# Kernel optimization log

Measured on AMD Instinct MI355X. Metric: run time of the kernel, lower is better.

Reference implementation:

```python
import jax, jax.numpy as jnp
import numpy as np

N_NODES = 19000   # STRING PPI nodes
N_EDGES = 600000  # avg degree ~32
B = 4096          # batch of perturbations
GNN = 256         # gnn_dim
H = 512           # hidden_dim
MID = 2048        # hidden_dim * expand
L = 6             # n_layers residual blocks
C = 3             # n_classes
R = 512           # bilinear_rank
G = 6640          # n_genes_out
LN_EPS = 1e-5


def _ln(x, scale, bias):
    mu = jnp.mean(x, axis=-1, keepdims=True)
    var = jnp.var(x, axis=-1, keepdims=True)
    return (x - mu) * jax.lax.rsqrt(var + LN_EPS) * scale + bias


def setup_inputs() -> dict:
    key = jax.random.key(0)
    ks = iter(jax.random.split(key, 24))
    s = lambda *sh: jax.random.normal(next(ks), sh, dtype=jnp.float32) * 0.02
    inp = {
        # -1 marks unknown genes (fallback embedding path)
        "node_indices": jax.random.randint(next(ks), (B,), -1, N_NODES),
        "edge_index": jax.random.randint(next(ks), (2, N_EDGES), 0, N_NODES),
        "edge_weight": jax.random.uniform(next(ks), (N_EDGES,), dtype=jnp.float32),
        # frozen mps.0-6 output cache (detached buffer in torch)
        "node_emb_cache": jax.random.normal(next(ks), (N_NODES, GNN), dtype=jnp.float32),
        # trainable graph tail (mps.7 modeled as GraphConv) + post_mp Linear
        "w_root": s(GNN, GNN),
        "w_neigh": s(GNN, GNN),
        "w_post": s(GNN, GNN),
        "b_post": jnp.zeros((GNN,), jnp.float32),
        "fallback_emb": s(GNN),
        # input_proj: LayerNorm(256) + Linear(256->512, no bias)
        "ln_in_scale": jnp.ones((GNN,), jnp.float32),
        "ln_in_bias": jnp.zeros((GNN,), jnp.float32),
        "w_in": s(H, GNN),
        # 6 residual blocks, stacked params
        "rb_ln_scale": jnp.ones((L, H), jnp.float32),
        "rb_ln_bias": jnp.zeros((L, H), jnp.float32),
        "rb_fc1": s(L, MID, H),
        "rb_fc2": s(L, H, MID),
        # bilinear head
        "w_bilinear": s(C * R, H),
        "out_gene_emb": s(G, R),
    }
    return inp


def reference(node_indices, edge_index, edge_weight, node_emb_cache,
              w_root, w_neigh, w_post, b_post, fallback_emb,
              ln_in_scale, ln_in_bias, w_in,
              rb_ln_scale, rb_ln_bias, rb_fc1, rb_fc2,
              w_bilinear, out_gene_emb):
    # --- trainable graph tail: mps.7 (GraphConv) + post_mp ---
    src, dst = edge_index[0], edge_index[1]
    msg = node_emb_cache[src] * edge_weight[:, None]          # [E, GNN]
    agg = jax.ops.segment_sum(msg, dst, num_segments=N_NODES)  # [N, GNN]
    x = jax.nn.relu(node_emb_cache @ w_root.T + agg @ w_neigh.T)
    node_emb = x @ w_post.T + b_post                           # [N, GNN]

    # --- gather perturbation embeddings with fallback for -1 ---
    known = node_indices >= 0
    safe = jnp.clip(node_indices, 0, None)
    pert = jnp.where(known[:, None], node_emb[safe], fallback_emb[None, :])  # [B, GNN]

    # --- input_proj + 6 residual blocks (dropout inactive in eval) ---
    h = _ln(pert, ln_in_scale, ln_in_bias) @ w_in.T            # [B, H]
    for i in range(L):
        y = _ln(h, rb_ln_scale[i], rb_ln_bias[i])
        y = jax.nn.gelu(y @ rb_fc1[i].T, approximate=False)    # exact erf GELU (torch default)
        h = y @ rb_fc2[i].T + h

    # --- bilinear head ---
    blin = (h @ w_bilinear.T).reshape(-1, C, R)                # [B, 3, R]
    logits = jnp.einsum('bcr,gr->bcg', blin, out_gene_emb)     # [B, 3, G]
    return logits
```

## Files before the change

kernel.cpp:

```cpp
#include <hip/hip_runtime.h>
#include <hip/hip_bf16.h>

#define N_NODES 19000
#define N_EDGES 600000
#define BATCH   4096
#define GNN_D   256
#define H_D     512
#define MID_D   2048
#define L_N     6
#define C_N     3
#define R_D     512
#define G_N     6640
#define LN_EPS  1e-5f
#define MAXDEG  128

typedef __attribute__((ext_vector_type(8))) short short8;
typedef __attribute__((ext_vector_type(4))) float f32x4;
typedef __hip_bfloat16 bf16;

#define SEG0 32768
#define SEG1 (SEG0 + 1572864)
#define SEG2 (SEG1 + 1572864)
#define SEG3 (SEG2 + 196608)
#define SEG4 (SEG3 + 849920)
#define SEG5 (SEG4 + 16384)
#define SEG6 (SEG5 + 32768)
#define CONV_TOT SEG6

__global__ void convert_weights_kernel(
    const float* __restrict__ w_in, const float* __restrict__ fc1,
    const float* __restrict__ fc2, const float* __restrict__ wbil,
    const float* __restrict__ gene, const float* __restrict__ wpost,
    const float* __restrict__ wroot, const float* __restrict__ wneigh,
    bf16* __restrict__ o_win, bf16* __restrict__ o_fc1, bf16* __restrict__ o_fc2,
    bf16* __restrict__ o_wbil, bf16* __restrict__ o_gene, bf16* __restrict__ o_wpost,
    bf16* __restrict__ o_wrn) {
  int i = blockIdx.x * blockDim.x + threadIdx.x;
  if (i >= CONV_TOT) return;
  const float* src;
  bf16* dst;
  if (i < SEG0)      { src = w_in  + (size_t)i * 4;            dst = o_win  + (size_t)i * 4; }
  else if (i < SEG1) { size_t j = i - SEG0; src = fc1  + j * 4; dst = o_fc1  + j * 4; }
  else if (i < SEG2) { size_t j = i - SEG1; src = fc2  + j * 4; dst = o_fc2  + j * 4; }
  else if (i < SEG3) { size_t j = i - SEG2; src = wbil + j * 4; dst = o_wbil + j * 4; }
  else if (i < SEG4) { size_t j = i - SEG3; src = gene + j * 4; dst = o_gene + j * 4; }
  else if (i < SEG5) { size_t j = i - SEG4; src = wpost+ j * 4; dst = o_wpost+ j * 4; }
  else {
    int j = i - SEG5;
    int base = j * 4;
    int n = base >> 9;
    int k = base & 511;
    src = (k < GNN_D) ? (wroot + (size_t)n * GNN_D + k)
                      : (wneigh + (size_t)n * GNN_D + (k - GNN_D));
    dst = o_wrn + base;
  }
  float4 v = *(const float4*)src;
  dst[0] = __float2bfloat16(v.x);
  dst[1] = __float2bfloat16(v.y);
  dst[2] = __float2bfloat16(v.z);
  dst[3] = __float2bfloat16(v.w);
}


__global__ void init_meta_kernel(int* __restrict__ flags, int* __restrict__ cursor,
                                 int* __restrict__ nuniq) {
  int i = blockIdx.x * blockDim.x + threadIdx.x;
  if (i < N_NODES) flags[i] = 0;
  if (i < BATCH) cursor[i] = 0;
  if (i == 0) *nuniq = 0;
}

__global__ void mark_needed_kernel(const int* __restrict__ idx, int* __restrict__ flags) {
  int i = blockIdx.x * blockDim.x + threadIdx.x;
  if (i < BATCH) {
    int id = idx[i];
    if (id >= 0) flags[id] = 1;
  }
}

__global__ void assign_slots_kernel(const int* __restrict__ flags, int* __restrict__ slot,
                                    int* __restrict__ uniq, int* __restrict__ nuniq) {
  int i = blockIdx.x * blockDim.x + threadIdx.x;
  if (i >= N_NODES) return;
  if (flags[i]) {
    int s = atomicAdd(nuniq, 1);
    slot[i] = s;
    uniq[s] = i;
  }
}

__global__ __launch_bounds__(256) void fill_edges_kernel(
    const int* __restrict__ ei, const float* __restrict__ ew,
    const int* __restrict__ flags, const int* __restrict__ slot,
    int* __restrict__ cursor, int* __restrict__ el_src, float* __restrict__ el_w) {
  int e = blockIdx.x * blockDim.x + threadIdx.x;
  if (e >= N_EDGES) return;
  int dst = ei[N_EDGES + e];
  if (!flags[dst]) return;
  int s = slot[dst];
  int p = atomicAdd(&cursor[s], 1);
  if (p < MAXDEG) {
    el_src[s * MAXDEG + p] = ei[e];
    el_w[s * MAXDEG + p] = ew[e];
  }
}

__global__ __launch_bounds__(256) void gather_nodes_kernel(
    const float* __restrict__ cache, const int* __restrict__ uniq,
    const int* __restrict__ cursor, const int* __restrict__ nuniq,
    const int* __restrict__ el_src, const float* __restrict__ el_w,
    bf16* __restrict__ compact2) {
  int s = blockIdx.x, t = threadIdx.x;
  bf16* row = compact2 + (size_t)s * (2 * GNN_D);
  if (s >= *nuniq) {
    row[t] = __float2bfloat16(0.f);
    row[GNN_D + t] = __float2bfloat16(0.f);
    return;
  }
  row[t] = __float2bfloat16(cache[(size_t)uniq[s] * GNN_D + t]);
  int deg = cursor[s];
  deg = (deg < MAXDEG) ? deg : MAXDEG;
  float acc = 0.f;
  for (int e = 0; e < deg; ++e) {
    int src = el_src[s * MAXDEG + e];
    float w = el_w[s * MAXDEG + e];
    acc += cache[(size_t)src * GNN_D + t] * w;
  }
  row[GNN_D + t] = __float2bfloat16(acc);
}

__global__ __launch_bounds__(256) void gather_ln_kernel(
    const float* __restrict__ embc, const int* __restrict__ slot,
    const float* __restrict__ fallback, const int* __restrict__ idx,
    const float* __restrict__ scale, const float* __restrict__ bias,
    bf16* __restrict__ out) {
  int b = blockIdx.x, t = threadIdx.x;
  int id = idx[b];
  float v = (id >= 0) ? embc[(size_t)slot[id] * GNN_D + t] : fallback[t];
  float s = v, q = v * v;
#pragma unroll
  for (int o = 32; o > 0; o >>= 1) { s += __shfl_down(s, o); q += __shfl_down(q, o); }
  __shared__ float ls[4], lq[4];
  int wv = t >> 6, ln = t & 63;
  if (ln == 0) { ls[wv] = s; lq[wv] = q; }
  __syncthreads();
  s = ls[0] + ls[1] + ls[2] + ls[3];
  q = lq[0] + lq[1] + lq[2] + lq[3];
  float mu = s * (1.f / GNN_D);
  float var = q * (1.f / GNN_D) - mu * mu;
  float r = rsqrtf(var + LN_EPS);
  out[(size_t)b * GNN_D + t] = __float2bfloat16((v - mu) * r * scale[t] + bias[t]);
}

__global__ __launch_bounds__(256) void ln512_kernel(
    const float* __restrict__ x, const float* __restrict__ scale,
    const float* __restrict__ bias, bf16* __restrict__ out) {
  int b = blockIdx.x, t = threadIdx.x;
  const float* xr = x + (size_t)b * H_D;
  float v0 = xr[t];
  float v1 = xr[256 + t];
  float s = v0 + v1, q = v0 * v0 + v1 * v1;
#pragma unroll
  for (int o = 32; o > 0; o >>= 1) { s += __shfl_down(s, o); q += __shfl_down(q, o); }
  __shared__ float ls[4], lq[4];
  int wv = t >> 6, ln = t & 63;
  if (ln == 0) { ls[wv] = s; lq[wv] = q; }
  __syncthreads();
  s = ls[0] + ls[1] + ls[2] + ls[3];
  q = lq[0] + lq[1] + lq[2] + lq[3];
  float mu = s * (1.f / H_D);
  float var = q * (1.f / H_D) - mu * mu;
  float r = rsqrtf(var + LN_EPS);
  bf16* orow = out + (size_t)b * H_D;
  orow[t]       = __float2bfloat16((v0 - mu) * r * scale[t]       + bias[t]);
  orow[256 + t] = __float2bfloat16((v1 - mu) * r * scale[256 + t] + bias[256 + t]);
}

__device__ inline float gelu_exact(float x) {
  return 0.5f * x * (1.f + erff(x * 0.70710678118654752f));
}


template <int WR, int WC, int NBM, int NBN, int ACT, int OUT_BF16, int ADDC, int BIAS,
          int HBF, int SWZ>
__global__ __launch_bounds__(WR * WC * 64) void gemm_mfma_kernel(
    const bf16* __restrict__ A, const bf16* __restrict__ W,
    const float* __restrict__ bias, const float* __restrict__ addC,
    void* __restrict__ Cout, bf16* __restrict__ out2,
    int M, int N, int K, int gx) {
  constexpr int THREADS = WR * WC * 64;
  constexpr int BM = NBM * 64;
  constexpr int BN = NBN * 64;
  constexpr int MR = BM / (WR * 16);
  constexpr int NR = BN / (WC * 16);
  constexpr int ITA = (BM * 4) / THREADS;
  constexpr int ITB = (BN * 4) / THREADS;
  __shared__ __align__(16) bf16 sA[2][BM * 32];
  __shared__ __align__(16) bf16 sB[2][BN * 32];
  const int tid = threadIdx.x;
  const int lane = tid & 63;
  const int wid = tid >> 6;
  const int wr = wid / WC, wc = wid % WC;

  int bidx, bidy;
  if (SWZ) {
    int nwg = gridDim.x;
    int bid = blockIdx.x;
    int l = (bid & 7) * (nwg >> 3) + (bid >> 3);
    bidx = l % gx;
    bidy = l / gx;
  } else {
    bidx = blockIdx.x;
    bidy = blockIdx.y;
  }
  const int bm = bidx * BM, bn = bidy * BN;

  f32x4 acc[MR][NR];
#pragma unroll
  for (int m = 0; m < MR; ++m)
#pragma unroll
    for (int n = 0; n < NR; ++n) acc[m][n] = (f32x4){0.f, 0.f, 0.f, 0.f};

  const int rbase = lane & 15;
  const int g = lane >> 4;
  const int kq = (tid & 3) << 3;

  int arow[ITA], brow[ITB];
#pragma unroll
  for (int i = 0; i < ITA; ++i) {
    int r0 = bm + ((i * THREADS + tid) >> 2);
    arow[i] = (r0 < M) ? r0 : (M - 1);
  }
#pragma unroll
  for (int i = 0; i < ITB; ++i) {
    int r0 = bn + ((i * THREADS + tid) >> 2);
    brow[i] = (r0 < N) ? r0 : (N - 1);
  }

  auto stage = [&](int buf, int k0) {
#pragma unroll
    for (int i = 0; i < ITA; ++i)
      __builtin_amdgcn_global_load_lds(
          (const __attribute__((address_space(1))) void*)(A + (size_t)arow[i] * K + k0 + kq),
          (__attribute__((address_space(3))) void*)(&sA[buf][(i * THREADS + tid) * 8]), 16, 0, 0);
#pragma unroll
    for (int i = 0; i < ITB; ++i)
      __builtin_amdgcn_global_load_lds(
          (const __attribute__((address_space(1))) void*)(W + (size_t)brow[i] * K + k0 + kq),
          (__attribute__((address_space(3))) void*)(&sB[buf][(i * THREADS + tid) * 8]), 16, 0, 0);
  };

  const int NT = K >> 5;
  stage(0, 0);
  __syncthreads();

  int cur = 0;
  for (int t = 0; t < NT; ++t) {
    if (t + 1 < NT) stage(cur ^ 1, (t + 1) << 5);

    short8 af[MR], bfrag[NR];
#pragma unroll
    for (int m = 0; m < MR; ++m)
      af[m] = *(const short8*)(&sA[cur][(wr * (BM / WR) + m * 16 + rbase) * 32 + g * 8]);
#pragma unroll
    for (int n = 0; n < NR; ++n)
      bfrag[n] = *(const short8*)(&sB[cur][(wc * (BN / WC) + n * 16 + rbase) * 32 + g * 8]);
#pragma unroll
    for (int m = 0; m < MR; ++m)
#pragma unroll
      for (int n = 0; n < NR; ++n)
        acc[m][n] = __builtin_amdgcn_mfma_f32_16x16x32_bf16(af[m], bfrag[n], acc[m][n], 0, 0, 0);

    __syncthreads();
    cur ^= 1;
  }

  const int rb = (lane >> 4) * 4;
  const int cb = lane & 15;
#pragma unroll
  for (int m = 0; m < MR; ++m) {
#pragma unroll
    for (int n = 0; n < NR; ++n) {
      int col = bn + wc * (BN / WC) + n * 16 + cb;
      if (col >= N) continue;
      int row0 = bm + wr * (BM / WR) + m * 16 + rb;
#pragma unroll
      for (int r = 0; r < 4; ++r) {
        int row = row0 + r;
        if (row >= M) continue;
        float v = acc[m][n][r];
        if (BIAS) v += bias[col];
        if (ADDC) v += addC[(size_t)row * N + col];
        if (ACT == 1) v = fmaxf(v, 0.f);
        if (ACT == 2) v = gelu_exact(v);
        if (OUT_BF16)
          ((bf16*)Cout)[(size_t)row * N + col] = __float2bfloat16(v);
        else
          ((float*)Cout)[(size_t)row * N + col] = v;
        if (HBF)
          out2[(size_t)row * N + col] = __float2bfloat16(v);
      }
    }
  }
}

template <int WR, int WC, int NBM, int NBN, int ACT, int OUT_BF16, int ADDC, int BIAS, int HBF>
static void launch_mfma(const bf16* A, const bf16* W, const float* bias,
                        const float* addC, void* C, bf16* out2,
                        int M, int N, int K, hipStream_t stream) {
  dim3 grid(M / (NBM * 64), (N + NBN * 64 - 1) / (NBN * 64));
  gemm_mfma_kernel<WR, WC, NBM, NBN, ACT, OUT_BF16, ADDC, BIAS, HBF, 0>
      <<<grid, WR * WC * 64, 0, stream>>>(A, W, bias, addC, C, out2, M, N, K, 0);
}


#define MB (1024u * 1024u)

extern "C" void kernel_launch(void* const* d_in, const int* in_sizes, int n_in,
                              void* d_out, int out_size, void* d_ws, size_t ws_size,
                              hipStream_t stream) {
  const int*   node_indices = (const int*)d_in[0];
  const int*   edge_index   = (const int*)d_in[1];
  const float* edge_weight  = (const float*)d_in[2];
  const float* cache        = (const float*)d_in[3];
  const float* w_root       = (const float*)d_in[4];
  const float* w_neigh      = (const float*)d_in[5];
  const float* w_post       = (const float*)d_in[6];
  const float* b_post       = (const float*)d_in[7];
  const float* fallback     = (const float*)d_in[8];
  const float* ln_in_scale  = (const float*)d_in[9];
  const float* ln_in_bias   = (const float*)d_in[10];
  const float* w_in         = (const float*)d_in[11];
  const float* rb_ln_scale  = (const float*)d_in[12];
  const float* rb_ln_bias   = (const float*)d_in[13];
  const float* rb_fc1       = (const float*)d_in[14];
  const float* rb_fc2       = (const float*)d_in[15];
  const float* w_bil        = (const float*)d_in[16];
  const float* gene         = (const float*)d_in[17];
  float* out = (float*)d_out;

  char* w = (char*)d_ws;
  bf16*  compact2 = (bf16*)(w + 0 * MB);
  bf16*  tmpc     = (bf16*)(w + 4 * MB);
  float* embc     = (float*)(w + 6 * MB);
  int*   el_src   = (int*)  (w + 10 * MB);
  float* el_w     = (float*)(w + 12 * MB);
  int*   flags    = (int*)  (w + 14 * MB);
  int*   slot     = (int*)  (w + 14 * MB + 80 * 1024);
  int*   uniq     = (int*)  (w + 14 * MB + 160 * 1024);
  int*   cursor   = (int*)  (w + 14 * MB + 180 * 1024);
  int*   nuniq    = (int*)  (w + 14 * MB + 200 * 1024);
  bf16*  ymid     = (bf16*) (w + 0 * MB);
  bf16*  pertln  = (bf16*) (w + 24 * MB);
  float* h       = (float*)(w + 26 * MB);
  bf16*  yln     = (bf16*) (w + 34 * MB);
  bf16*  h_bf    = (bf16*) (w + 38 * MB);
  bf16*  blin    = (bf16*) (w + 42 * MB);
  bf16*  w_in_bf = (bf16*) (w + 55 * MB);
  bf16*  fc1_bf  = (bf16*) (w + 56 * MB);
  bf16*  fc2_bf  = (bf16*) (w + 68 * MB);
  bf16*  wbil_bf = (bf16*) (w + 80 * MB);
  bf16*  gene_bf = (bf16*) (w + 82 * MB);
  bf16*  wrn_bf  = (bf16*) (w + 90 * MB);
  bf16*  wpost_bf= (bf16*) (w + 91 * MB);

  convert_weights_kernel<<<(CONV_TOT + 255) / 256, 256, 0, stream>>>(
      w_in, rb_fc1, rb_fc2, w_bil, gene, w_post, w_root, w_neigh,
      w_in_bf, fc1_bf, fc2_bf, wbil_bf, gene_bf, wpost_bf, wrn_bf);

  init_meta_kernel<<<(N_NODES + 255) / 256, 256, 0, stream>>>(flags, cursor, nuniq);
  mark_needed_kernel<<<(BATCH + 255) / 256, 256, 0, stream>>>(node_indices, flags);
  assign_slots_kernel<<<(N_NODES + 255) / 256, 256, 0, stream>>>(flags, slot, uniq, nuniq);
  fill_edges_kernel<<<(N_EDGES + 255) / 256, 256, 0, stream>>>(
      edge_index, edge_weight, flags, slot, cursor, el_src, el_w);
  gather_nodes_kernel<<<BATCH, 256, 0, stream>>>(
      cache, uniq, cursor, nuniq, el_src, el_w, compact2);

  launch_mfma<2, 2, 1, 1, 1, 1, 0, 0, 0>(compact2, wrn_bf, nullptr, nullptr, tmpc, nullptr,
                                         BATCH, GNN_D, 2 * GNN_D, stream);
  launch_mfma<2, 2, 1, 1, 0, 0, 0, 1, 0>(tmpc, wpost_bf, b_post, nullptr, embc, nullptr,
                                         BATCH, GNN_D, GNN_D, stream);

  gather_ln_kernel<<<BATCH, 256, 0, stream>>>(embc, slot, fallback, node_indices,
                                              ln_in_scale, ln_in_bias, pertln);
  launch_mfma<2, 2, 1, 1, 0, 0, 0, 0, 0>(pertln, w_in_bf, nullptr, nullptr, h, nullptr,
                                         BATCH, H_D, GNN_D, stream);

  for (int i = 0; i < L_N; ++i) {
    ln512_kernel<<<BATCH, 256, 0, stream>>>(h, rb_ln_scale + (size_t)i * H_D,
                                            rb_ln_bias + (size_t)i * H_D, yln);
    launch_mfma<2, 2, 2, 2, 2, 1, 0, 0, 0>(yln, fc1_bf + (size_t)i * MID_D * H_D,
                                           nullptr, nullptr, ymid, nullptr,
                                           BATCH, MID_D, H_D, stream);
    if (i < L_N - 1)
      launch_mfma<2, 2, 1, 1, 0, 0, 1, 0, 0>(ymid, fc2_bf + (size_t)i * H_D * MID_D,
                                             nullptr, h, h, nullptr,
                                             BATCH, H_D, MID_D, stream);
    else
      launch_mfma<2, 2, 1, 1, 0, 0, 1, 0, 1>(ymid, fc2_bf + (size_t)i * H_D * MID_D,
                                             nullptr, h, h, h_bf,
                                             BATCH, H_D, MID_D, stream);
  }

  launch_mfma<2, 2, 1, 2, 0, 1, 0, 0, 0>(h_bf, wbil_bf, nullptr, nullptr, blin, nullptr,
                                         BATCH, C_N * R_D, H_D, stream);
  {
    int gx = (BATCH * C_N) / 256;
    int gy = (G_N + 255) / 256;
    int nwg = gx * gy;
    gemm_mfma_kernel<2, 4, 4, 4, 0, 0, 0, 0, 0, 1><<<nwg, 512, 0, stream>>>(
        blin, gene_bf, nullptr, nullptr, out, nullptr, BATCH * C_N, G_N, R_D, gx);
  }
}
```

Measured before the change: 627.2 us.

## Fuse residual-block LayerNorm into fc1 GEMM via epilogue row statistics

Removes the standalone ln512 kernels. The producing GEMMs (input projection and fc2) now accumulate per-row sum and sum-of-squares in their epilogue with shuffles and atomics. The fc1 GEMM then normalizes fp32 h on the fly while staging its A tile into LDS. This saves six launches and the bf16 LN round trip, but fc1's A staging becomes synchronous register loads of fp32 (twice the bytes) instead of async global_load_lds. It also adds atomic traffic and a single-pass variance formula.

After: 663.0 us. 1.06x slower.

```diff
diff --git a/kernel.cpp b/kernel.cpp
--- a/kernel.cpp
+++ b/kernel.cpp
@@ -63,11 +63,17 @@
 
 
 __global__ void init_meta_kernel(int* __restrict__ flags, int* __restrict__ cursor,
-                                 int* __restrict__ nuniq) {
+                                 int* __restrict__ nuniq, float* __restrict__ rowstat) {
   int i = blockIdx.x * blockDim.x + threadIdx.x;
   if (i < N_NODES) flags[i] = 0;
   if (i < BATCH) cursor[i] = 0;
   if (i == 0) *nuniq = 0;
+  const int RS_TOT = 6 * BATCH * 2;
+#pragma unroll
+  for (int j = 0; j < 3; ++j) {
+    int k = i * 3 + j;
+    if (k < RS_TOT) rowstat[k] = 0.f;
+  }
 }
 
 __global__ void mark_needed_kernel(const int* __restrict__ idx, int* __restrict__ flags) {
@@ -152,41 +158,20 @@
   out[(size_t)b * GNN_D + t] = __float2bfloat16((v - mu) * r * scale[t] + bias[t]);
 }
 
-__global__ __launch_bounds__(256) void ln512_kernel(
-    const float* __restrict__ x, const float* __restrict__ scale,
-    const float* __restrict__ bias, bf16* __restrict__ out) {
-  int b = blockIdx.x, t = threadIdx.x;
-  const float* xr = x + (size_t)b * H_D;
-  float v0 = xr[t];
-  float v1 = xr[256 + t];
-  float s = v0 + v1, q = v0 * v0 + v1 * v1;
-#pragma unroll
-  for (int o = 32; o > 0; o >>= 1) { s += __shfl_down(s, o); q += __shfl_down(q, o); }
-  __shared__ float ls[4], lq[4];
-  int wv = t >> 6, ln = t & 63;
-  if (ln == 0) { ls[wv] = s; lq[wv] = q; }
-  __syncthreads();
-  s = ls[0] + ls[1] + ls[2] + ls[3];
-  q = lq[0] + lq[1] + lq[2] + lq[3];
-  float mu = s * (1.f / H_D);
-  float var = q * (1.f / H_D) - mu * mu;
-  float r = rsqrtf(var + LN_EPS);
-  bf16* orow = out + (size_t)b * H_D;
-  orow[t]       = __float2bfloat16((v0 - mu) * r * scale[t]       + bias[t]);
-  orow[256 + t] = __float2bfloat16((v1 - mu) * r * scale[256 + t] + bias[256 + t]);
-}
-
 __device__ inline float gelu_exact(float x) {
   return 0.5f * x * (1.f + erff(x * 0.70710678118654752f));
 }
 
 
 template <int WR, int WC, int NBM, int NBN, int ACT, int OUT_BF16, int ADDC, int BIAS,
-          int HBF, int SWZ>
+          int HBF, int SWZ, int STATS, int LNA>
 __global__ __launch_bounds__(WR * WC * 64) void gemm_mfma_kernel(
     const bf16* __restrict__ A, const bf16* __restrict__ W,
     const float* __restrict__ bias, const float* __restrict__ addC,
     void* __restrict__ Cout, bf16* __restrict__ out2,
+    const float* __restrict__ Af32, const float* __restrict__ rs_in,
+    const float* __restrict__ ln_sc, const float* __restrict__ ln_bi,
+    float* __restrict__ rs_out,
     int M, int N, int K, int gx) {
   constexpr int THREADS = WR * WC * 64;
   constexpr int BM = NBM * 64;
@@ -237,12 +222,51 @@
     brow[i] = (r0 < N) ? r0 : (N - 1);
   }
 
-  auto stage = [&](int buf, int k0) {
-#pragma unroll
-    for (int i = 0; i < ITA; ++i)
-      __builtin_amdgcn_global_load_lds(
-          (const __attribute__((address_space(1))) void*)(A + (size_t)arow[i] * K + k0 + kq),
-          (__attribute__((address_space(3))) void*)(&sA[buf][(i * THREADS + tid) * 8]), 16, 0, 0);
+  float mu_i[ITA], rs_i[ITA];
+  if constexpr (LNA) {
+#pragma unroll
+    for (int i = 0; i < ITA; ++i) {
+      float s = rs_in[arow[i] * 2];
+      float q = rs_in[arow[i] * 2 + 1];
+      float mu = s * (1.f / (float)K);
+      float var = q * (1.f / (float)K) - mu * mu;
+      mu_i[i] = mu;
+      rs_i[i] = rsqrtf(var + LN_EPS);
+    }
+  }
+
+  auto stageA = [&](int buf, int k0) {
+    if constexpr (LNA) {
+#pragma unroll
+      for (int i = 0; i < ITA; ++i) {
+        const float* hp = Af32 + (size_t)arow[i] * K + k0 + kq;
+        float4 u0 = *(const float4*)(hp);
+        float4 u1 = *(const float4*)(hp + 4);
+        float4 s0 = *(const float4*)(ln_sc + k0 + kq);
+        float4 s1 = *(const float4*)(ln_sc + k0 + kq + 4);
+        float4 b0 = *(const float4*)(ln_bi + k0 + kq);
+        float4 b1 = *(const float4*)(ln_bi + k0 + kq + 4);
+        float mu = mu_i[i], rs = rs_i[i];
+        bf16 o[8];
+        o[0] = __float2bfloat16((u0.x - mu) * rs * s0.x + b0.x);
+        o[1] = __float2bfloat16((u0.y - mu) * rs * s0.y + b0.y);
+        o[2] = __float2bfloat16((u0.z - mu) * rs * s0.z + b0.z);
+        o[3] = __float2bfloat16((u0.w - mu) * rs * s0.w + b0.w);
+        o[4] = __float2bfloat16((u1.x - mu) * rs * s1.x + b1.x);
+        o[5] = __float2bfloat16((u1.y - mu) * rs * s1.y + b1.y);
+        o[6] = __float2bfloat16((u1.z - mu) * rs * s1.z + b1.z);
+        o[7] = __float2bfloat16((u1.w - mu) * rs * s1.w + b1.w);
+        *(short8*)(&sA[buf][(i * THREADS + tid) * 8]) = *(const short8*)o;
+      }
+    } else {
+#pragma unroll
+      for (int i = 0; i < ITA; ++i)
+        __builtin_amdgcn_global_load_lds(
+            (const __attribute__((address_space(1))) void*)(A + (size_t)arow[i] * K + k0 + kq),
+            (__attribute__((address_space(3))) void*)(&sA[buf][(i * THREADS + tid) * 8]), 16, 0, 0);
+    }
+  };
+  auto stageB = [&](int buf, int k0) {
 #pragma unroll
     for (int i = 0; i < ITB; ++i)
       __builtin_amdgcn_global_load_lds(
@@ -251,12 +275,13 @@
   };
 
   const int NT = K >> 5;
-  stage(0, 0);
+  stageA(0, 0);
+  stageB(0, 0);
   __syncthreads();
 
   int cur = 0;
   for (int t = 0; t < NT; ++t) {
-    if (t + 1 < NT) stage(cur ^ 1, (t + 1) << 5);
+    if (t + 1 < NT) { stageA(cur ^ 1, (t + 1) << 5); stageB(cur ^ 1, (t + 1) << 5); }
 
     short8 af[MR], bfrag[NR];
 #pragma unroll
@@ -277,6 +302,13 @@
 
   const int rb = (lane >> 4) * 4;
   const int cb = lane & 15;
+  float ps[MR][4], pq[MR][4];
+  if constexpr (STATS) {
+#pragma unroll
+    for (int m = 0; m < MR; ++m)
+#pragma unroll
+      for (int r = 0; r < 4; ++r) { ps[m][r] = 0.f; pq[m][r] = 0.f; }
+  }
 #pragma unroll
   for (int m = 0; m < MR; ++m) {
 #pragma unroll
@@ -293,6 +325,7 @@
         if (ADDC) v += addC[(size_t)row * N + col];
         if (ACT == 1) v = fmaxf(v, 0.f);
         if (ACT == 2) v = gelu_exact(v);
+        if (STATS) { ps[m][r] += v; pq[m][r] += v * v; }
         if (OUT_BF16)
           ((bf16*)Cout)[(size_t)row * N + col] = __float2bfloat16(v);
         else
@@ -302,15 +335,35 @@
       }
     }
   }
-}
-
-template <int WR, int WC, int NBM, int NBN, int ACT, int OUT_BF16, int ADDC, int BIAS, int HBF>
+  if constexpr (STATS) {
+#pragma unroll
+    for (int m = 0; m < MR; ++m) {
+#pragma unroll
+      for (int r = 0; r < 4; ++r) {
+        float s = ps[m][r], q = pq[m][r];
+#pragma unroll
+        for (int o = 1; o < 16; o <<= 1) { s += __shfl_xor(s, o); q += __shfl_xor(q, o); }
+        if ((lane & 15) == 0) {
+          int row = bm + wr * (BM / WR) + m * 16 + rb + r;
+          atomicAdd(&rs_out[row * 2], s);
+          atomicAdd(&rs_out[row * 2 + 1], q);
+        }
+      }
+    }
+  }
+}
+
+template <int WR, int WC, int NBM, int NBN, int ACT, int OUT_BF16, int ADDC, int BIAS,
+          int HBF, int STATS, int LNA>
 static void launch_mfma(const bf16* A, const bf16* W, const float* bias,
                         const float* addC, void* C, bf16* out2,
+                        const float* Af32, const float* rs_in,
+                        const float* ln_sc, const float* ln_bi, float* rs_out,
                         int M, int N, int K, hipStream_t stream) {
   dim3 grid(M / (NBM * 64), (N + NBN * 64 - 1) / (NBN * 64));
-  gemm_mfma_kernel<WR, WC, NBM, NBN, ACT, OUT_BF16, ADDC, BIAS, HBF, 0>
-      <<<grid, WR * WC * 64, 0, stream>>>(A, W, bias, addC, C, out2, M, N, K, 0);
+  gemm_mfma_kernel<WR, WC, NBM, NBN, ACT, OUT_BF16, ADDC, BIAS, HBF, 0, STATS, LNA>
+      <<<grid, WR * WC * 64, 0, stream>>>(A, W, bias, addC, C, out2,
+                                          Af32, rs_in, ln_sc, ln_bi, rs_out, M, N, K, 0);
 }
 
 
@@ -353,7 +406,6 @@
   bf16*  ymid     = (bf16*) (w + 0 * MB);
   bf16*  pertln  = (bf16*) (w + 24 * MB);
   float* h       = (float*)(w + 26 * MB);
-  bf16*  yln     = (bf16*) (w + 34 * MB);
   bf16*  h_bf    = (bf16*) (w + 38 * MB);
   bf16*  blin    = (bf16*) (w + 42 * MB);
   bf16*  w_in_bf = (bf16*) (w + 55 * MB);
@@ -363,12 +415,13 @@
   bf16*  gene_bf = (bf16*) (w + 82 * MB);
   bf16*  wrn_bf  = (bf16*) (w + 90 * MB);
   bf16*  wpost_bf= (bf16*) (w + 91 * MB);
+  float* rowstat = (float*)(w + 92 * MB);
 
   convert_weights_kernel<<<(CONV_TOT + 255) / 256, 256, 0, stream>>>(
       w_in, rb_fc1, rb_fc2, w_bil, gene, w_post, w_root, w_neigh,
       w_in_bf, fc1_bf, fc2_bf, wbil_bf, gene_bf, wpost_bf, wrn_bf);
 
-  init_meta_kernel<<<(N_NODES + 255) / 256, 256, 0, stream>>>(flags, cursor, nuniq);
+  init_meta_kernel<<<(N_NODES + 255) / 256, 256, 0, stream>>>(flags, cursor, nuniq, rowstat);
   mark_needed_kernel<<<(BATCH + 255) / 256, 256, 0, stream>>>(node_indices, flags);
   assign_slots_kernel<<<(N_NODES + 255) / 256, 256, 0, stream>>>(flags, slot, uniq, nuniq);
   fill_edges_kernel<<<(N_EDGES + 255) / 256, 256, 0, stream>>>(
@@ -376,39 +429,46 @@
   gather_nodes_kernel<<<BATCH, 256, 0, stream>>>(
       cache, uniq, cursor, nuniq, el_src, el_w, compact2);
 
-  launch_mfma<2, 2, 1, 1, 1, 1, 0, 0, 0>(compact2, wrn_bf, nullptr, nullptr, tmpc, nullptr,
-                                         BATCH, GNN_D, 2 * GNN_D, stream);
-  launch_mfma<2, 2, 1, 1, 0, 0, 0, 1, 0>(tmpc, wpost_bf, b_post, nullptr, embc, nullptr,
-                                         BATCH, GNN_D, GNN_D, stream);
+  launch_mfma<2, 2, 1, 1, 1, 1, 0, 0, 0, 0, 0>(
+      compact2, wrn_bf, nullptr, nullptr, tmpc, nullptr,
+      nullptr, nullptr, nullptr, nullptr, nullptr, BATCH, GNN_D, 2 * GNN_D, stream);
+  launch_mfma<2, 2, 1, 1, 0, 0, 0, 1, 0, 0, 0>(
+      tmpc, wpost_bf, b_post, nullptr, embc, nullptr,
+      nullptr, nullptr, nullptr, nullptr, nullptr, BATCH, GNN_D, GNN_D, stream);
 
   gather_ln_kernel<<<BATCH, 256, 0, stream>>>(embc, slot, fallback, node_indices,
                                               ln_in_scale, ln_in_bias, pertln);
-  launch_mfma<2, 2, 1, 1, 0, 0, 0, 0, 0>(pertln, w_in_bf, nullptr, nullptr, h, nullptr,
-                                         BATCH, H_D, GNN_D, stream);
+  launch_mfma<2, 2, 1, 1, 0, 0, 0, 0, 0, 1, 0>(
+      pertln, w_in_bf, nullptr, nullptr, h, nullptr,
+      nullptr, nullptr, nullptr, nullptr, rowstat, BATCH, H_D, GNN_D, stream);
 
   for (int i = 0; i < L_N; ++i) {
-    ln512_kernel<<<BATCH, 256, 0, stream>>>(h, rb_ln_scale + (size_t)i * H_D,
-                                            rb_ln_bias + (size_t)i * H_D, yln);
-    launch_mfma<2, 2, 2, 2, 2, 1, 0, 0, 0>(yln, fc1_bf + (size_t)i * MID_D * H_D,
-                                           nullptr, nullptr, ymid, nullptr,
-                                           BATCH, MID_D, H_D, stream);
+    launch_mfma<2, 2, 2, 2, 2, 1, 0, 0, 0, 0, 1>(
+        nullptr, fc1_bf + (size_t)i * MID_D * H_D, nullptr, nullptr, ymid, nullptr,
+        h, rowstat + (size_t)i * BATCH * 2,
+        rb_ln_scale + (size_t)i * H_D, rb_ln_bias + (size_t)i * H_D, nullptr,
+        BATCH, MID_D, H_D, stream);
     if (i < L_N - 1)
-      launch_mfma<2, 2, 1, 1, 0, 0, 1, 0, 0>(ymid, fc2_bf + (size_t)i * H_D * MID_D,
-                                             nullptr, h, h, nullptr,
-                                             BATCH, H_D, MID_D, stream);
+      launch_mfma<2, 2, 1, 1, 0, 0, 1, 0, 0, 1, 0>(
+          ymid, fc2_bf + (size_t)i * H_D * MID_D, nullptr, h, h, nullptr,
+          nullptr, nullptr, nullptr, nullptr, rowstat + (size_t)(i + 1) * BATCH * 2,
+          BATCH, H_D, MID_D, stream);
     else
-      launch_mfma<2, 2, 1, 1, 0, 0, 1, 0, 1>(ymid, fc2_bf + (size_t)i * H_D * MID_D,
-                                             nullptr, h, h, h_bf,
-                                             BATCH, H_D, MID_D, stream);
-  }
-
-  launch_mfma<2, 2, 1, 2, 0, 1, 0, 0, 0>(h_bf, wbil_bf, nullptr, nullptr, blin, nullptr,
-                                         BATCH, C_N * R_D, H_D, stream);
+      launch_mfma<2, 2, 1, 1, 0, 0, 1, 0, 1, 0, 0>(
+          ymid, fc2_bf + (size_t)i * H_D * MID_D, nullptr, h, h, h_bf,
+          nullptr, nullptr, nullptr, nullptr, nullptr,
+          BATCH, H_D, MID_D, stream);
+  }
+
+  launch_mfma<2, 2, 1, 2, 0, 1, 0, 0, 0, 0, 0>(
+      h_bf, wbil_bf, nullptr, nullptr, blin, nullptr,
+      nullptr, nullptr, nullptr, nullptr, nullptr, BATCH, C_N * R_D, H_D, stream);
   {
     int gx = (BATCH * C_N) / 256;
     int gy = (G_N + 255) / 256;
     int nwg = gx * gy;
-    gemm_mfma_kernel<2, 4, 4, 4, 0, 0, 0, 0, 0, 1><<<nwg, 512, 0, stream>>>(
-        blin, gene_bf, nullptr, nullptr, out, nullptr, BATCH * C_N, G_N, R_D, gx);
-  }
-}
+    gemm_mfma_kernel<2, 4, 4, 4, 0, 0, 0, 0, 0, 1, 0, 0><<<nwg, 512, 0, stream>>>(
+        blin, gene_bf, nullptr, nullptr, out, nullptr,
+        nullptr, nullptr, nullptr, nullptr, nullptr, BATCH * C_N, G_N, R_D, gx);
+  }
+}
```
